# Optimization experiments

Hardware: AMD Instinct MI355X
Metric: run time of the kernel (lower is better)

The kernel has to match this reference:

```python
import jax, jax.numpy as jnp
import numpy as np

B, T, C, H = 16, 2048, 1024, 64

def setup_inputs() -> dict:
    key = jax.random.key(0)
    kx, kq, kk, kv = jax.random.split(key, 4)
    x = jax.random.normal(kx, (B, T, C), dtype=jnp.float32)
    Wq = jax.random.normal(kq, (C, H), dtype=jnp.float32) * (C ** -0.5)
    Wk = jax.random.normal(kk, (C, H), dtype=jnp.float32) * (C ** -0.5)
    Wv = jax.random.normal(kv, (C, H), dtype=jnp.float32) * (C ** -0.5)
    return {"x": x, "Wq": Wq, "Wk": Wk, "Wv": Wv}

def reference(x, Wq, Wk, Wv):
    # single causal self-attention head; dropout p=0.0 (identity)
    Tlen = x.shape[1]
    q = jnp.einsum('btc,ch->bth', x, Wq)  # [B,T,H]
    k = jnp.einsum('btc,ch->bth', x, Wk)
    v = jnp.einsum('btc,ch->bth', x, Wv)
    scale = q.shape[-1] ** -0.5
    scores = jnp.einsum('bth,bsh->bts', q, k) * scale  # [B,T,T]
    causal = jnp.tril(jnp.ones((Tlen, Tlen), dtype=bool))
    scores = jnp.where(causal, scores, -jnp.inf)
    weights = jax.nn.softmax(scores, axis=-1)
    out = jnp.einsum('bts,bsh->bth', weights, v)  # [B,T,H]
    return out
```

## Files before the change

### kernel.cpp

```cpp
#include <hip/hip_runtime.h>


typedef float  floatx4 __attribute__((ext_vector_type(4)));
typedef __bf16 bf16x8  __attribute__((ext_vector_type(8)));
typedef short  short8v __attribute__((ext_vector_type(8)));
typedef unsigned short ushort4v __attribute__((ext_vector_type(4)));

constexpr int Bn = 16;
constexpr int Tn = 2048;
constexpr int Cn = 1024;
constexpr int Hn = 64;
constexpr int BT = Bn * Tn;

#define QSCALE 0.1803368867f

__device__ __forceinline__ unsigned short f2b(float f) {
  unsigned int u = __builtin_bit_cast(unsigned int, f);
  u += 0x7fffu + ((u >> 16) & 1u);
  return (unsigned short)(u >> 16);
}

__global__ __launch_bounds__(256) void pack_w(const float* __restrict__ Wq,
                                              const float* __restrict__ Wk,
                                              const float* __restrict__ Wv,
                                              unsigned short* __restrict__ Wp) {
  int gid = blockIdx.x * 256 + threadIdx.x;
  int mat = gid >> 16;
  int rem = gid & 65535;
  int k   = rem >> 6;
  int col = rem & 63;
  const float* W = (mat == 0) ? Wq : (mat == 1) ? Wk : Wv;
  float v = W[rem];
  int kb = k >> 3, j = k & 7, ct = (mat << 2) | (col >> 4), c = col & 15;
  size_t idx = ((((size_t)ct * 128) + kb) * 16 + c) * 8 + j;
  Wp[idx] = f2b(v);
}

__global__ __launch_bounds__(256) void proj_kernel(
    const float* __restrict__ x, const unsigned short* __restrict__ Wp,
    unsigned short* __restrict__ Q, unsigned short* __restrict__ K,
    unsigned short* __restrict__ Vt) {
  __shared__ alignas(16) unsigned short Al[2][64][72];

  const int tid  = threadIdx.x;
  const int wave = tid >> 6;
  const int lane = tid & 63;
  const int quad = lane >> 4;
  const int l16  = lane & 15;
  const int wr   = wave >> 1;
  const int wc   = wave & 1;
  const int rbase = blockIdx.x * 64;

  floatx4 acc[2][6];
#pragma unroll
  for (int a = 0; a < 2; ++a)
#pragma unroll
    for (int b = 0; b < 6; ++b) acc[a][b] = (floatx4){0.f, 0.f, 0.f, 0.f};

  const int arow = tid >> 2;
  const int acol = (tid & 3) * 16;
  const float* xp = x + (size_t)(rbase + arow) * Cn + acol;

  floatx4 f0 = *reinterpret_cast<const floatx4*>(xp);
  floatx4 f1 = *reinterpret_cast<const floatx4*>(xp + 4);
  floatx4 f2 = *reinterpret_cast<const floatx4*>(xp + 8);
  floatx4 f3 = *reinterpret_cast<const floatx4*>(xp + 12);

  for (int k0 = 0; k0 < Cn; k0 += 64) {
    const int buf = (k0 >> 6) & 1;

    short8v p0, p1;
    p0[0] = (short)f2b(f0[0]); p0[1] = (short)f2b(f0[1]);
    p0[2] = (short)f2b(f0[2]); p0[3] = (short)f2b(f0[3]);
    p0[4] = (short)f2b(f1[0]); p0[5] = (short)f2b(f1[1]);
    p0[6] = (short)f2b(f1[2]); p0[7] = (short)f2b(f1[3]);
    p1[0] = (short)f2b(f2[0]); p1[1] = (short)f2b(f2[1]);
    p1[2] = (short)f2b(f2[2]); p1[3] = (short)f2b(f2[3]);
    p1[4] = (short)f2b(f3[0]); p1[5] = (short)f2b(f3[1]);
    p1[6] = (short)f2b(f3[2]); p1[7] = (short)f2b(f3[3]);
    *reinterpret_cast<short8v*>(&Al[buf][arow][acol])     = p0;
    *reinterpret_cast<short8v*>(&Al[buf][arow][acol + 8]) = p1;

    __syncthreads();

    if (k0 + 64 < Cn) {
      f0 = *reinterpret_cast<const floatx4*>(xp + k0 + 64);
      f1 = *reinterpret_cast<const floatx4*>(xp + k0 + 68);
      f2 = *reinterpret_cast<const floatx4*>(xp + k0 + 72);
      f3 = *reinterpret_cast<const floatx4*>(xp + k0 + 76);
    }

#pragma unroll
    for (int kk = 0; kk < 2; ++kk) {
      bf16x8 a0 = *reinterpret_cast<const bf16x8*>(
          &Al[buf][wr * 32 + l16][kk * 32 + quad * 8]);
      bf16x8 a1 = *reinterpret_cast<const bf16x8*>(
          &Al[buf][wr * 32 + 16 + l16][kk * 32 + quad * 8]);
#pragma unroll
      for (int c6 = 0; c6 < 6; ++c6) {
        const int ct = wc * 6 + c6;
        bf16x8 bfr = *reinterpret_cast<const bf16x8*>(
            Wp + ((size_t)(ct * 128 + (k0 >> 3) + kk * 4 + quad) * 16 + l16) * 8);
        acc[0][c6] = __builtin_amdgcn_mfma_f32_16x16x32_bf16(a0, bfr, acc[0][c6], 0, 0, 0);
        acc[1][c6] = __builtin_amdgcn_mfma_f32_16x16x32_bf16(a1, bfr, acc[1][c6], 0, 0, 0);
      }
    }
  }

#pragma unroll
  for (int rt = 0; rt < 2; ++rt) {
#pragma unroll
    for (int c6 = 0; c6 < 6; ++c6) {
      const int cbase  = wc * 96 + c6 * 16;
      const int rowloc = wr * 32 + rt * 16 + quad * 4;
      if (cbase < 64) {
#pragma unroll
        for (int r = 0; r < 4; ++r)
          Q[(size_t)(rbase + rowloc + r) * Hn + cbase + l16] =
              f2b(acc[rt][c6][r] * QSCALE);
      } else if (cbase < 128) {
#pragma unroll
        for (int r = 0; r < 4; ++r)
          K[(size_t)(rbase + rowloc + r) * Hn + cbase - 64 + l16] =
              f2b(acc[rt][c6][r]);
      } else {
        const int b  = rbase >> 11;
        const int t0 = (rbase & 2047) + rowloc;
        const int h  = cbase - 128 + l16;
        ushort4v v;
#pragma unroll
        for (int r = 0; r < 4; ++r) v[r] = f2b(acc[rt][c6][r]);
        *reinterpret_cast<ushort4v*>(&Vt[((size_t)b * Hn + h) * Tn + t0]) = v;
      }
    }
  }
}

__global__ __launch_bounds__(256) void flash_kernel(
    const unsigned short* __restrict__ Q, const unsigned short* __restrict__ K,
    const unsigned short* __restrict__ Vt, float* __restrict__ out) {
  __shared__ alignas(16) unsigned short P[4][16][72];
  __shared__ alignas(16) float Om[4][16][68];
  __shared__ float Ll[4][16];

  const int tid  = threadIdx.x;
  const int wave = tid >> 6;
  const int lane = tid & 63;
  const int quad = lane >> 4;
  const int l16  = lane & 15;

  const int b   = blockIdx.x & 15;
  const int p16 = 127 - (blockIdx.x >> 4);
  const int qbase = p16 * 16;
  const int n_tiles  = (p16 >> 2) + 1;
  const int lastTile = p16 >> 2;
  const size_t bbase  = (size_t)b * Tn * Hn;
  const size_t vtbase = (size_t)b * Hn * Tn;

  bf16x8 qf[2];
#pragma unroll
  for (int i = 0; i < 2; ++i)
    qf[i] = *reinterpret_cast<const bf16x8*>(
        &Q[bbase + (size_t)(qbase + l16) * Hn + i * 32 + quad * 8]);

  floatx4 O[4];
#pragma unroll
  for (int i = 0; i < 4; ++i) O[i] = (floatx4){0.f, 0.f, 0.f, 0.f};
  float l_r[4] = {0.f, 0.f, 0.f, 0.f};

  for (int kt = wave; kt < n_tiles; kt += 4) {
    const int kvbase = kt * 64;

    floatx4 S[4];
#pragma unroll
    for (int ct = 0; ct < 4; ++ct) {
      floatx4 s = (floatx4){0.f, 0.f, 0.f, 0.f};
#pragma unroll
      for (int kk = 0; kk < 2; ++kk) {
        bf16x8 bfr = *reinterpret_cast<const bf16x8*>(
            &K[bbase + (size_t)(kvbase + ct * 16 + l16) * Hn + kk * 32 + quad * 8]);
        s = __builtin_amdgcn_mfma_f32_16x16x32_bf16(qf[kk], bfr, s, 0, 0, 0);
      }
      S[ct] = s;
    }

    bf16x8 vf[4][2];
#pragma unroll
    for (int ht = 0; ht < 4; ++ht)
#pragma unroll
      for (int kk = 0; kk < 2; ++kk)
        vf[ht][kk] = *reinterpret_cast<const bf16x8*>(
            &Vt[vtbase + (size_t)(ht * 16 + l16) * Tn + kvbase + kk * 32 + quad * 8]);

    if (kt == lastTile) {
#pragma unroll
      for (int ct = 0; ct < 4; ++ct)
#pragma unroll
        for (int r = 0; r < 4; ++r) {
          int trow = qbase + quad * 4 + r;
          int scol = kvbase + ct * 16 + l16;
          if (scol > trow) S[ct][r] = -1e30f;
        }
    }

#pragma unroll
    for (int r = 0; r < 4; ++r) {
      float p0 = __builtin_amdgcn_exp2f(S[0][r]);
      float p1 = __builtin_amdgcn_exp2f(S[1][r]);
      float p2 = __builtin_amdgcn_exp2f(S[2][r]);
      float p3 = __builtin_amdgcn_exp2f(S[3][r]);
      l_r[r] += (p0 + p1) + (p2 + p3);
      P[wave][quad * 4 + r][l16]      = f2b(p0);
      P[wave][quad * 4 + r][16 + l16] = f2b(p1);
      P[wave][quad * 4 + r][32 + l16] = f2b(p2);
      P[wave][quad * 4 + r][48 + l16] = f2b(p3);
    }

    bf16x8 pf0 = *reinterpret_cast<const bf16x8*>(&P[wave][l16][quad * 8]);
    bf16x8 pf1 = *reinterpret_cast<const bf16x8*>(&P[wave][l16][32 + quad * 8]);
#pragma unroll
    for (int ht = 0; ht < 4; ++ht) {
      O[ht] = __builtin_amdgcn_mfma_f32_16x16x32_bf16(pf0, vf[ht][0], O[ht], 0, 0, 0);
      O[ht] = __builtin_amdgcn_mfma_f32_16x16x32_bf16(pf1, vf[ht][1], O[ht], 0, 0, 0);
    }
  }

#pragma unroll
  for (int r = 0; r < 4; ++r)
#pragma unroll
    for (int d = 1; d < 16; d <<= 1) l_r[r] += __shfl_xor(l_r[r], d);

#pragma unroll
  for (int ht = 0; ht < 4; ++ht)
#pragma unroll
    for (int r = 0; r < 4; ++r)
      Om[wave][quad * 4 + r][ht * 16 + l16] = O[ht][r];
  if (l16 == 0) {
#pragma unroll
    for (int r = 0; r < 4; ++r) Ll[wave][quad * 4 + r] = l_r[r];
  }
  __syncthreads();

  {
    const int row = tid >> 4;
    const int c4  = (tid & 15) * 4;
    float L = (Ll[0][row] + Ll[1][row]) + (Ll[2][row] + Ll[3][row]);
    float invL = 1.0f / L;
    floatx4 o0 = *reinterpret_cast<const floatx4*>(&Om[0][row][c4]);
    floatx4 o1 = *reinterpret_cast<const floatx4*>(&Om[1][row][c4]);
    floatx4 o2 = *reinterpret_cast<const floatx4*>(&Om[2][row][c4]);
    floatx4 o3 = *reinterpret_cast<const floatx4*>(&Om[3][row][c4]);
    floatx4 res;
#pragma unroll
    for (int j = 0; j < 4; ++j)
      res[j] = ((o0[j] + o1[j]) + (o2[j] + o3[j])) * invL;
    *reinterpret_cast<floatx4*>(
        &out[bbase + (size_t)(qbase + row) * Hn + c4]) = res;
  }
}

extern "C" void kernel_launch(void* const* d_in, const int* in_sizes, int n_in,
                              void* d_out, int out_size, void* d_ws, size_t ws_size,
                              hipStream_t stream) {
  const float* x  = (const float*)d_in[0];
  const float* Wq = (const float*)d_in[1];
  const float* Wk = (const float*)d_in[2];
  const float* Wv = (const float*)d_in[3];
  float* out = (float*)d_out;

  char* ws = (char*)d_ws;
  unsigned short* Q  = (unsigned short*)(ws);
  unsigned short* Kb = (unsigned short*)(ws + ((size_t)4 << 20));
  unsigned short* Vt = (unsigned short*)(ws + ((size_t)8 << 20));
  unsigned short* Wp = (unsigned short*)(ws + ((size_t)12 << 20));

  pack_w<<<dim3(768), dim3(256), 0, stream>>>(Wq, Wk, Wv, Wp);
  proj_kernel<<<dim3(BT / 64), dim3(256), 0, stream>>>(x, Wp, Q, Kb, Vt);
  flash_kernel<<<dim3(16 * 128), dim3(256), 0, stream>>>(Q, Kb, Vt, out);
}
```

Before: 280.6 us.

## Rewrite projection as single-wave blocks loading x fragments directly without LDS

The projection kernel changes from 256-thread blocks that stage 64 rows of x through a double-buffered shared tile into 64-thread blocks that each handle 32 rows. Each lane loads its MFMA A fragment straight from global memory, converts it to bf16 in registers, and computes all 12 output column tiles. This removes LDS traffic and block barriers. In exchange, each wave now re-reads the full packed weight matrix with less reuse per load, holds twice as many accumulators, and reads x with a strided pattern.

```diff
diff --git a/kernel.cpp b/kernel.cpp
--- a/kernel.cpp
+++ b/kernel.cpp
@@ -18,6 +18,15 @@
   unsigned int u = __builtin_bit_cast(unsigned int, f);
   u += 0x7fffu + ((u >> 16) & 1u);
   return (unsigned short)(u >> 16);
+}
+
+__device__ __forceinline__ bf16x8 cvt8(floatx4 a, floatx4 b) {
+  short8v p;
+  p[0] = (short)f2b(a[0]); p[1] = (short)f2b(a[1]);
+  p[2] = (short)f2b(a[2]); p[3] = (short)f2b(a[3]);
+  p[4] = (short)f2b(b[0]); p[5] = (short)f2b(b[1]);
+  p[6] = (short)f2b(b[2]); p[7] = (short)f2b(b[3]);
+  return __builtin_bit_cast(bf16x8, p);
 }
 
 __global__ __launch_bounds__(256) void pack_w(const float* __restrict__ Wq,
@@ -36,101 +45,74 @@
   Wp[idx] = f2b(v);
 }
 
-__global__ __launch_bounds__(256) void proj_kernel(
+__global__ __launch_bounds__(64) void proj_kernel(
     const float* __restrict__ x, const unsigned short* __restrict__ Wp,
     unsigned short* __restrict__ Q, unsigned short* __restrict__ K,
     unsigned short* __restrict__ Vt) {
-  __shared__ alignas(16) unsigned short Al[2][64][72];
-
-  const int tid  = threadIdx.x;
-  const int wave = tid >> 6;
-  const int lane = tid & 63;
+  const int lane = threadIdx.x;
   const int quad = lane >> 4;
   const int l16  = lane & 15;
-  const int wr   = wave >> 1;
-  const int wc   = wave & 1;
-  const int rbase = blockIdx.x * 64;
-
-  floatx4 acc[2][6];
+  const int rbase = blockIdx.x * 32;
+
+  floatx4 acc[2][12];
 #pragma unroll
   for (int a = 0; a < 2; ++a)
 #pragma unroll
-    for (int b = 0; b < 6; ++b) acc[a][b] = (floatx4){0.f, 0.f, 0.f, 0.f};
-
-  const int arow = tid >> 2;
-  const int acol = (tid & 3) * 16;
-  const float* xp = x + (size_t)(rbase + arow) * Cn + acol;
-
-  floatx4 f0 = *reinterpret_cast<const floatx4*>(xp);
-  floatx4 f1 = *reinterpret_cast<const floatx4*>(xp + 4);
-  floatx4 f2 = *reinterpret_cast<const floatx4*>(xp + 8);
-  floatx4 f3 = *reinterpret_cast<const floatx4*>(xp + 12);
-
-  for (int k0 = 0; k0 < Cn; k0 += 64) {
-    const int buf = (k0 >> 6) & 1;
-
-    short8v p0, p1;
-    p0[0] = (short)f2b(f0[0]); p0[1] = (short)f2b(f0[1]);
-    p0[2] = (short)f2b(f0[2]); p0[3] = (short)f2b(f0[3]);
-    p0[4] = (short)f2b(f1[0]); p0[5] = (short)f2b(f1[1]);
-    p0[6] = (short)f2b(f1[2]); p0[7] = (short)f2b(f1[3]);
-    p1[0] = (short)f2b(f2[0]); p1[1] = (short)f2b(f2[1]);
-    p1[2] = (short)f2b(f2[2]); p1[3] = (short)f2b(f2[3]);
-    p1[4] = (short)f2b(f3[0]); p1[5] = (short)f2b(f3[1]);
-    p1[6] = (short)f2b(f3[2]); p1[7] = (short)f2b(f3[3]);
-    *reinterpret_cast<short8v*>(&Al[buf][arow][acol])     = p0;
-    *reinterpret_cast<short8v*>(&Al[buf][arow][acol + 8]) = p1;
-
-    __syncthreads();
-
-    if (k0 + 64 < Cn) {
-      f0 = *reinterpret_cast<const floatx4*>(xp + k0 + 64);
-      f1 = *reinterpret_cast<const floatx4*>(xp + k0 + 68);
-      f2 = *reinterpret_cast<const floatx4*>(xp + k0 + 72);
-      f3 = *reinterpret_cast<const floatx4*>(xp + k0 + 76);
-    }
-
-#pragma unroll
-    for (int kk = 0; kk < 2; ++kk) {
-      bf16x8 a0 = *reinterpret_cast<const bf16x8*>(
-          &Al[buf][wr * 32 + l16][kk * 32 + quad * 8]);
-      bf16x8 a1 = *reinterpret_cast<const bf16x8*>(
-          &Al[buf][wr * 32 + 16 + l16][kk * 32 + quad * 8]);
-#pragma unroll
-      for (int c6 = 0; c6 < 6; ++c6) {
-        const int ct = wc * 6 + c6;
-        bf16x8 bfr = *reinterpret_cast<const bf16x8*>(
-            Wp + ((size_t)(ct * 128 + (k0 >> 3) + kk * 4 + quad) * 16 + l16) * 8);
-        acc[0][c6] = __builtin_amdgcn_mfma_f32_16x16x32_bf16(a0, bfr, acc[0][c6], 0, 0, 0);
-        acc[1][c6] = __builtin_amdgcn_mfma_f32_16x16x32_bf16(a1, bfr, acc[1][c6], 0, 0, 0);
-      }
-    }
-  }
-
+    for (int t = 0; t < 12; ++t) acc[a][t] = (floatx4){0.f, 0.f, 0.f, 0.f};
+
+  const float* xr0 = x + (size_t)(rbase + l16) * Cn + quad * 8;
+  const float* xr1 = x + (size_t)(rbase + 16 + l16) * Cn + quad * 8;
+
+  floatx4 a00 = *reinterpret_cast<const floatx4*>(xr0);
+  floatx4 a01 = *reinterpret_cast<const floatx4*>(xr0 + 4);
+  floatx4 a10 = *reinterpret_cast<const floatx4*>(xr1);
+  floatx4 a11 = *reinterpret_cast<const floatx4*>(xr1 + 4);
+
+  for (int s = 0; s < 32; ++s) {
+    bf16x8 af0 = cvt8(a00, a01);
+    bf16x8 af1 = cvt8(a10, a11);
+
+    if (s < 31) {
+      const int koff = (s + 1) * 32;
+      a00 = *reinterpret_cast<const floatx4*>(xr0 + koff);
+      a01 = *reinterpret_cast<const floatx4*>(xr0 + koff + 4);
+      a10 = *reinterpret_cast<const floatx4*>(xr1 + koff);
+      a11 = *reinterpret_cast<const floatx4*>(xr1 + koff + 4);
+    }
+
+    const unsigned short* wb = Wp + (size_t)(s * 4 + quad) * 128 + l16 * 8;
+#pragma unroll
+    for (int t = 0; t < 12; ++t) {
+      bf16x8 bfr = *reinterpret_cast<const bf16x8*>(wb + t * 16384);
+      acc[0][t] = __builtin_amdgcn_mfma_f32_16x16x32_bf16(af0, bfr, acc[0][t], 0, 0, 0);
+      acc[1][t] = __builtin_amdgcn_mfma_f32_16x16x32_bf16(af1, bfr, acc[1][t], 0, 0, 0);
+    }
+  }
+
+  const int b  = rbase >> 11;
+  const int tb = rbase & 2047;
 #pragma unroll
   for (int rt = 0; rt < 2; ++rt) {
-#pragma unroll
-    for (int c6 = 0; c6 < 6; ++c6) {
-      const int cbase  = wc * 96 + c6 * 16;
-      const int rowloc = wr * 32 + rt * 16 + quad * 4;
-      if (cbase < 64) {
+    const int rowloc = rt * 16 + quad * 4;
+#pragma unroll
+    for (int ct = 0; ct < 12; ++ct) {
+      if (ct < 4) {
 #pragma unroll
         for (int r = 0; r < 4; ++r)
-          Q[(size_t)(rbase + rowloc + r) * Hn + cbase + l16] =
-              f2b(acc[rt][c6][r] * QSCALE);
-      } else if (cbase < 128) {
+          Q[(size_t)(rbase + rowloc + r) * Hn + ct * 16 + l16] =
+              f2b(acc[rt][ct][r] * QSCALE);
+      } else if (ct < 8) {
 #pragma unroll
         for (int r = 0; r < 4; ++r)
-          K[(size_t)(rbase + rowloc + r) * Hn + cbase - 64 + l16] =
-              f2b(acc[rt][c6][r]);
+          K[(size_t)(rbase + rowloc + r) * Hn + (ct - 4) * 16 + l16] =
+              f2b(acc[rt][ct][r]);
       } else {
-        const int b  = rbase >> 11;
-        const int t0 = (rbase & 2047) + rowloc;
-        const int h  = cbase - 128 + l16;
+        const int h = (ct - 8) * 16 + l16;
         ushort4v v;
 #pragma unroll
-        for (int r = 0; r < 4; ++r) v[r] = f2b(acc[rt][c6][r]);
-        *reinterpret_cast<ushort4v*>(&Vt[((size_t)b * Hn + h) * Tn + t0]) = v;
+        for (int r = 0; r < 4; ++r) v[r] = f2b(acc[rt][ct][r]);
+        *reinterpret_cast<ushort4v*>(
+            &Vt[((size_t)b * Hn + h) * Tn + tb + rowloc]) = v;
       }
     }
   }
@@ -275,6 +257,6 @@
   unsigned short* Wp = (unsigned short*)(ws + ((size_t)12 << 20));
 
   pack_w<<<dim3(768), dim3(256), 0, stream>>>(Wq, Wk, Wv, Wp);
-  proj_kernel<<<dim3(BT / 64), dim3(256), 0, stream>>>(x, Wp, Q, Kb, Vt);
+  proj_kernel<<<dim3(BT / 32), dim3(64), 0, stream>>>(x, Wp, Q, Kb, Vt);
   flash_kernel<<<dim3(16 * 128), dim3(256), 0, stream>>>(Q, Kb, Vt, out);
 }
```

New measurement: 285.3 us. No clear change (+1.7%).
